# Optimization experiments

Hardware: AMD Instinct MI355X
Metric: run time of the kernel (lower is better)

## Reference

```python
import jax, jax.numpy as jnp
import numpy as np

EPS = 1e-06

def rmsnorm(x, w):
    x32 = x.astype(jnp.float32)
    var = jnp.mean(x32 * x32, axis=-1, keepdims=True)
    return w * (x32 * jax.lax.rsqrt(var + EPS)).astype(x.dtype)

def setup_inputs() -> dict:
    B, T, C = 16, 256, 16
    token_dim, text_dim = 1024, 512
    key = jax.random.key(0)
    ks = jax.random.split(key, 8)
    token_embeds = jax.random.normal(ks[0], (B, T, token_dim), dtype=jnp.float32)
    char_embeds = jax.random.normal(ks[1], (B, T, C, text_dim), dtype=jnp.float32)
    filler_embed = jax.random.normal(ks[2], (text_dim,), dtype=jnp.float32)
    mask = jax.random.randint(ks[3], (B, T, C), 0, 2).astype(bool)
    mask = mask.at[0].set(True)  # force max valid count == T*C (static output shape)
    token_ids_mask = jnp.ones((B, T), dtype=bool)
    # xavier-uniform-ish weights
    def xav(k, fan_out, fan_in, gain=1.0):
        lim = gain * np.sqrt(6.0 / (fan_in + fan_out))
        return jax.random.uniform(k, (fan_out, fan_in), jnp.float32, -lim, lim)
    W_down = xav(ks[4], text_dim, token_dim)
    W_proj = xav(ks[5], 3, text_dim, gain=0.2)
    W_fusion = xav(ks[6], text_dim, text_dim)
    w_pre = jnp.ones((token_dim,), jnp.float32)
    w_tok = jnp.ones((text_dim,), jnp.float32)
    w_char = jnp.ones((text_dim,), jnp.float32)
    return {"token_embeds": token_embeds, "token_ids_mask": token_ids_mask,
            "char_embeds": char_embeds, "char_ids_mask": mask,
            "filler_embed": filler_embed, "w_pre": w_pre, "w_tok": w_tok,
            "w_char": w_char, "W_down": W_down, "W_proj": W_proj,
            "W_fusion": W_fusion, "max_valid_chars": T * C}

def reference(token_embeds, token_ids_mask, char_embeds, char_ids_mask,
              filler_embed, w_pre, w_tok, w_char, W_down, W_proj, W_fusion,
              max_valid_chars):
    B, T, C, d = char_embeds.shape
    MV = int(max_valid_chars)
    tok = rmsnorm(token_embeds, w_pre)                       # [B,T,token_dim]
    feats = rmsnorm(jnp.einsum('btk,dk->btd', tok, W_down), w_tok)  # [B,T,d]
    params = jnp.einsum('btd,pd->btp', jax.nn.silu(feats), W_proj)  # [B,T,3]
    scale = params[..., 0][:, :, None, None]                 # [B,T,1,1]
    shift = params[..., 1][:, :, None, None]
    gate = jax.nn.sigmoid(params[..., 2][:, :, None, None])
    cn = rmsnorm(char_embeds, w_char)                        # [B,T,C,d]
    fused = jnp.einsum('btcd,ed->btce', jax.nn.silu(cn * (1.0 + scale) + shift), W_fusion)
    fused = gate * fused + (1.0 - gate) * cn                 # [B,T,C,d]
    flat = fused.reshape(B, T * C, d)
    m = char_ids_mask.reshape(B, T * C).astype(jnp.int32)
    pos = jnp.cumsum(m, axis=1) - 1                          # dest within row
    offs = jnp.arange(B, dtype=jnp.int32)[:, None] * MV
    idx = jnp.where(m > 0, offs + pos, B * MV)               # invalid -> dump slot
    buf = jnp.broadcast_to(filler_embed, (B * MV + 1, d))
    buf = buf.at[idx.reshape(-1)].set(flat.reshape(-1, d))
    return buf[: B * MV].reshape(B, MV, d)
```

## Files before the change

kernel.cpp:

```cpp
#include <hip/hip_runtime.h>
#include <cstdint>
#include <cstddef>

#define EPS 1e-6f

typedef short bf16x8 __attribute__((ext_vector_type(8)));
typedef float f32x4  __attribute__((ext_vector_type(4)));

__device__ __forceinline__ short f2bf(float x) {
    uint32_t u = __builtin_bit_cast(uint32_t, x);
    return (short)((u + 0x7FFFu + ((u >> 16) & 1u)) >> 16);
}
__device__ __forceinline__ float bf2f(short s) {
    uint32_t u = ((uint32_t)(uint16_t)s) << 16;
    return __builtin_bit_cast(float, u);
}

__global__ __launch_bounds__(256) void k_scan(const void* __restrict__ maskp,
                                              int* __restrict__ v_list,
                                              int* __restrict__ counts) {
    __shared__ int sc[256];
    __shared__ int mode_s;
    const int tid = threadIdx.x;
    const int b = blockIdx.x;
    const uint32_t* mi = (const uint32_t*)maskp;

    if (tid == 0) mode_s = 0;
    __syncthreads();
    int bad = 0;
    for (int k = tid; k < 1024; k += 256) bad |= (mi[k] > 1u) ? 1 : 0;
    if (bad) mode_s = 1;
    __syncthreads();

    int m[16];
    if (mode_s) {
        const uint4 v = *(const uint4*)((const uint8_t*)maskp + (b << 12) + tid * 16);
        const uint32_t ws[4] = {v.x, v.y, v.z, v.w};
#pragma unroll
        for (int w4 = 0; w4 < 4; ++w4)
#pragma unroll
            for (int e = 0; e < 4; ++e)
                m[w4 * 4 + e] = ((ws[w4] >> (8 * e)) & 0xffu) ? 1 : 0;
    } else {
        const uint32_t* p = mi + (b << 12) + tid * 16;
#pragma unroll
        for (int q = 0; q < 16; ++q) m[q] = p[q] ? 1 : 0;
    }
    int cl = 0;
#pragma unroll
    for (int q = 0; q < 16; ++q) cl += m[q];
    sc[tid] = cl;
    __syncthreads();
    for (int off = 1; off < 256; off <<= 1) {
        int v = sc[tid];
        int a = (tid >= off) ? sc[tid - off] : 0;
        __syncthreads();
        sc[tid] = v + a;
        __syncthreads();
    }
    int pos = sc[tid] - cl;
#pragma unroll
    for (int q = 0; q < 16; ++q) {
        if (m[q]) v_list[(b << 12) + pos++] = tid * 16 + q;
    }
    if (tid == 255) counts[b] = sc[255];
}

__global__ __launch_bounds__(256) void k_conv2(
    const float* __restrict__ s1, short* __restrict__ d1, int n1,
    const float* __restrict__ s2, short* __restrict__ d2, int n2) {
    const int gid = blockIdx.x * 256 + threadIdx.x;
    const float* src; short* dst; int idx;
    if (gid < n1) { src = s1; dst = d1; idx = gid; }
    else if (gid < n1 + n2) { src = s2; dst = d2; idx = gid - n1; }
    else return;
    const float4 v = ((const float4*)src)[idx];
    short4 o;
    o.x = f2bf(v.x); o.y = f2bf(v.y); o.z = f2bf(v.z); o.w = f2bf(v.w);
    ((short4*)dst)[idx] = o;
}

__global__ __launch_bounds__(256) void k_tokprep(const float* __restrict__ tokens,
                                                 const float* __restrict__ w_pre,
                                                 short* __restrict__ tokbf) {
    const int tid = threadIdx.x, lane = tid & 63, wave = tid >> 6;
    const int row = blockIdx.x * 4 + wave;
    const float* xp = tokens + (size_t)row * 1024 + lane * 16;
    float4 x[4];
#pragma unroll
    for (int q = 0; q < 4; ++q) x[q] = *(const float4*)&xp[q * 4];
    float ss = 0.f;
#pragma unroll
    for (int q = 0; q < 4; ++q)
        ss += x[q].x * x[q].x + x[q].y * x[q].y + x[q].z * x[q].z + x[q].w * x[q].w;
#pragma unroll
    for (int off = 32; off > 0; off >>= 1) ss += __shfl_down(ss, off);
    ss = __shfl(ss, 0);
    const float r = rsqrtf(ss * (1.0f / 1024.0f) + EPS);
    const float* wp = w_pre + lane * 16;
    short* op = tokbf + (size_t)row * 1024 + lane * 16;
#pragma unroll
    for (int h = 0; h < 2; ++h) {
        bf16x8 o;
#pragma unroll
        for (int q = 0; q < 2; ++q) {
            const float4 wv = *(const float4*)&wp[h * 8 + q * 4];
            const float4 xv = x[h * 2 + q];
            o[q * 4 + 0] = f2bf(xv.x * wv.x * r);
            o[q * 4 + 1] = f2bf(xv.y * wv.y * r);
            o[q * 4 + 2] = f2bf(xv.z * wv.z * r);
            o[q * 4 + 3] = f2bf(xv.w * wv.w * r);
        }
        *(bf16x8*)&op[h * 8] = o;
    }
}

__global__ __launch_bounds__(256) void k_gemm_tok(const short* __restrict__ tokbf,
                                                  const short* __restrict__ Wdbf,
                                                  float* __restrict__ feats) {
    __shared__ short As[128 * 32];
    __shared__ short Bs[64 * 32];
    const int tid = threadIdx.x, lane = tid & 63, w = tid >> 6;
    const int mt = blockIdx.x >> 3, nt = blockIdx.x & 7;
    const int wm = w >> 1, wn = w & 1;
    const short* hA = tokbf + (size_t)mt * 128 * 1024;
    const short* wB = Wdbf + (size_t)nt * 64 * 1024;

    f32x4 acc[4][2];
#pragma unroll
    for (int mi = 0; mi < 4; ++mi)
#pragma unroll
        for (int ni = 0; ni < 2; ++ni) acc[mi][ni] = (f32x4)0.f;

    const int rA = lane & 15, q8 = (lane >> 4) * 8;
    for (int kk = 0; kk < 1024; kk += 32) {
#pragma unroll
        for (int q = 0; q < 2; ++q) {
            const int cid = (w * 2 + q) * 64 + lane;
            const int r = cid >> 2, kc = cid & 3;
            __builtin_amdgcn_global_load_lds(
                (const __attribute__((address_space(1))) uint32_t*)(hA + (size_t)r * 1024 + kk + kc * 8),
                (__attribute__((address_space(3))) uint32_t*)&As[(w * 2 + q) * 512], 16, 0, 0);
        }
        {
            const int cid = tid;
            const int r = cid >> 2, kc = cid & 3;
            __builtin_amdgcn_global_load_lds(
                (const __attribute__((address_space(1))) uint32_t*)(wB + (size_t)r * 1024 + kk + kc * 8),
                (__attribute__((address_space(3))) uint32_t*)&Bs[w * 512], 16, 0, 0);
        }
        __syncthreads();
        bf16x8 af[4], bfr[2];
#pragma unroll
        for (int mi = 0; mi < 4; ++mi)
            af[mi] = *(const bf16x8*)&As[(wm * 64 + mi * 16 + rA) * 32 + q8];
#pragma unroll
        for (int ni = 0; ni < 2; ++ni)
            bfr[ni] = *(const bf16x8*)&Bs[(wn * 32 + ni * 16 + rA) * 32 + q8];
#pragma unroll
        for (int mi = 0; mi < 4; ++mi)
#pragma unroll
            for (int ni = 0; ni < 2; ++ni)
                acc[mi][ni] = __builtin_amdgcn_mfma_f32_16x16x32_bf16(af[mi], bfr[ni], acc[mi][ni], 0, 0, 0);
        __syncthreads();
    }
    const int rowb = mt * 128 + wm * 64 + (lane >> 4) * 4;
    const int colb = nt * 64 + wn * 32 + (lane & 15);
#pragma unroll
    for (int mi = 0; mi < 4; ++mi)
#pragma unroll
        for (int ni = 0; ni < 2; ++ni)
#pragma unroll
            for (int rg = 0; rg < 4; ++rg)
                feats[(size_t)(rowb + mi * 16 + rg) * 512 + colb + ni * 16] = acc[mi][ni][rg];
}

__global__ __launch_bounds__(64) void k_params(
    const float* __restrict__ feats_pre, const float* __restrict__ w_tok,
    const float* __restrict__ W_proj, float* __restrict__ params) {
    const int tk = blockIdx.x;
    const int lane = threadIdx.x;
    const int d0 = lane * 8;
    const float* fp = feats_pre + (size_t)tk * 512 + d0;
    const float4 f0 = *(const float4*)&fp[0];
    const float4 f1 = *(const float4*)&fp[4];
    float ss = f0.x * f0.x + f0.y * f0.y + f0.z * f0.z + f0.w * f0.w
             + f1.x * f1.x + f1.y * f1.y + f1.z * f1.z + f1.w * f1.w;
#pragma unroll
    for (int off = 32; off > 0; off >>= 1) ss += __shfl_down(ss, off);
    ss = __shfl(ss, 0);
    const float rms = rsqrtf(ss * (1.0f / 512.0f) + EPS);

    const float4 wt0 = *(const float4*)&w_tok[d0];
    const float4 wt1 = *(const float4*)&w_tok[d0 + 4];
    float fv[8] = {f0.x, f0.y, f0.z, f0.w, f1.x, f1.y, f1.z, f1.w};
    float wv[8] = {wt0.x, wt0.y, wt0.z, wt0.w, wt1.x, wt1.y, wt1.z, wt1.w};
    float s[8];
#pragma unroll
    for (int j = 0; j < 8; ++j) {
        const float v = fv[j] * wv[j] * rms;
        s[j] = v / (1.0f + expf(-v));
    }
    float p[3];
#pragma unroll
    for (int q = 0; q < 3; ++q) {
        const float* Wp = W_proj + (size_t)q * 512 + d0;
        const float4 a = *(const float4*)&Wp[0];
        const float4 c = *(const float4*)&Wp[4];
        p[q] = s[0] * a.x + s[1] * a.y + s[2] * a.z + s[3] * a.w
             + s[4] * c.x + s[5] * c.y + s[6] * c.z + s[7] * c.w;
#pragma unroll
        for (int off = 32; off > 0; off >>= 1) p[q] += __shfl_down(p[q], off);
    }
    if (lane == 0) {
        float* po = params + (size_t)tk * 4;
        po[0] = 1.0f + p[0];
        po[1] = p[1];
        po[2] = 1.0f / (1.0f + expf(-p[2]));
    }
}

__global__ __launch_bounds__(256) void k_prep(
    const float* __restrict__ chars, const float* __restrict__ w_char,
    const float* __restrict__ params, const int* __restrict__ v_list,
    const int* __restrict__ counts, short* __restrict__ hb,
    short* __restrict__ cnp, float* __restrict__ g_l) {
    const int tid = threadIdx.x, lane = tid & 63, wave = tid >> 6;
    const int b = blockIdx.x >> 10;
    const int j = (blockIdx.x & 1023) * 4 + wave;
    const int cnt = counts[b];
    const int cpad = (cnt + 127) & ~127;
    if (j >= cpad) return;
    short* hrow = hb + ((size_t)(b << 12) + j) * 512 + lane * 8;
    if (j >= cnt) {
        *(bf16x8*)hrow = (bf16x8)0;
        return;
    }
    const int i = v_list[(b << 12) + j];
    const float* xp = chars + ((size_t)(b << 12) + i) * 512 + lane * 8;
    const float4 x0 = *(const float4*)&xp[0];
    const float4 x1 = *(const float4*)&xp[4];
    float ss = x0.x * x0.x + x0.y * x0.y + x0.z * x0.z + x0.w * x0.w
             + x1.x * x1.x + x1.y * x1.y + x1.z * x1.z + x1.w * x1.w;
#pragma unroll
    for (int off = 32; off > 0; off >>= 1) ss += __shfl_down(ss, off);
    ss = __shfl(ss, 0);
    const float rms = rsqrtf(ss * (1.0f / 512.0f) + EPS);
    const float* pp = params + (size_t)((b << 8) + (i >> 4)) * 4;
    const float s1 = pp[0], sh = pp[1], g = pp[2];
    const float4 w0 = *(const float4*)&w_char[lane * 8];
    const float4 w1 = *(const float4*)&w_char[lane * 8 + 4];
    float xv[8] = {x0.x, x0.y, x0.z, x0.w, x1.x, x1.y, x1.z, x1.w};
    float wv[8] = {w0.x, w0.y, w0.z, w0.w, w1.x, w1.y, w1.z, w1.w};
    bf16x8 oh, oc;
    const float gm1 = 1.0f - g;
#pragma unroll
    for (int q = 0; q < 8; ++q) {
        const float cn = wv[q] * xv[q] * rms;
        const float a = cn * s1 + sh;
        oh[q] = f2bf(a / (1.0f + expf(-a)));
        oc[q] = f2bf(gm1 * cn);
    }
    *(bf16x8*)hrow = oh;
    *(bf16x8*)(cnp + ((size_t)(b << 12) + j) * 512 + lane * 8) = oc;
    if (lane == 0) g_l[(b << 12) + j] = g;
}

__global__ __launch_bounds__(256) void k_fill(
    const float* __restrict__ filler, const int* __restrict__ counts,
    float* __restrict__ out) {
    const int gid = blockIdx.x * 256 + threadIdx.x;
    const size_t e4 = (size_t)gid * 4;
    const int slot = gid >> 7;
    const int b = slot >> 12;
    const int j = slot & 4095;
    if (j >= counts[b]) {
        const int e0 = (int)(e4 & 511);
        *(float4*)&out[e4] = *(const float4*)&filler[e0];
    }
}

__global__ __launch_bounds__(256) void k_gemm_fus(
    const short* __restrict__ hb, const short* __restrict__ Wbf,
    const short* __restrict__ cnp, const float* __restrict__ g_l,
    const int* __restrict__ counts, float* __restrict__ out) {
    __shared__ union SM {
        struct { short A[128 * 32]; short B[128 * 32]; } ab;
        float ep[32][132];
    } sm;
    __shared__ float g_s[128];
    const int tid = threadIdx.x, lane = tid & 63, w = tid >> 6;
    const int b = blockIdx.x >> 7;
    const int mt = (blockIdx.x >> 2) & 31;
    const int nt = blockIdx.x & 3;
    const int cnt = counts[b];
    const int row0 = mt * 128;
    if (row0 >= cnt) return;
    const int wm = w >> 1, wn = w & 1;

    if (tid < 128) {
        const int j = row0 + tid;
        g_s[tid] = (j < cnt) ? g_l[(b << 12) + j] : 0.f;
    }

    const short* hA = hb + ((size_t)(b << 12) + row0) * 512;
    const short* wB = Wbf + (size_t)nt * 128 * 512;

    f32x4 acc[4][4];
#pragma unroll
    for (int mi = 0; mi < 4; ++mi)
#pragma unroll
        for (int ni = 0; ni < 4; ++ni) acc[mi][ni] = (f32x4)0.f;

    const int rA = lane & 15, q8 = (lane >> 4) * 8;
    for (int kk = 0; kk < 512; kk += 32) {
#pragma unroll
        for (int q = 0; q < 2; ++q) {
            const int cid = (w * 2 + q) * 64 + lane;
            const int r = cid >> 2, kc = cid & 3;
            const size_t go = (size_t)r * 512 + kk + kc * 8;
            __builtin_amdgcn_global_load_lds(
                (const __attribute__((address_space(1))) uint32_t*)(hA + go),
                (__attribute__((address_space(3))) uint32_t*)&sm.ab.A[(w * 2 + q) * 512], 16, 0, 0);
            __builtin_amdgcn_global_load_lds(
                (const __attribute__((address_space(1))) uint32_t*)(wB + go),
                (__attribute__((address_space(3))) uint32_t*)&sm.ab.B[(w * 2 + q) * 512], 16, 0, 0);
        }
        __syncthreads();
        bf16x8 af[4], bfr[4];
#pragma unroll
        for (int mi = 0; mi < 4; ++mi)
            af[mi] = *(const bf16x8*)&sm.ab.A[(wm * 64 + mi * 16 + rA) * 32 + q8];
#pragma unroll
        for (int ni = 0; ni < 4; ++ni)
            bfr[ni] = *(const bf16x8*)&sm.ab.B[(wn * 64 + ni * 16 + rA) * 32 + q8];
#pragma unroll
        for (int mi = 0; mi < 4; ++mi)
#pragma unroll
            for (int ni = 0; ni < 4; ++ni)
                acc[mi][ni] = __builtin_amdgcn_mfma_f32_16x16x32_bf16(af[mi], bfr[ni], acc[mi][ni], 0, 0, 0);
        __syncthreads();
    }

    const int r5 = tid >> 3;
    const int c0 = (tid & 7) * 16;
    const int cg = nt * 128 + c0;
#pragma unroll
    for (int mi = 0; mi < 4; ++mi) {
#pragma unroll
        for (int ni = 0; ni < 4; ++ni)
#pragma unroll
            for (int rg = 0; rg < 4; ++rg)
                sm.ep[wm * 16 + (lane >> 4) * 4 + rg][wn * 64 + ni * 16 + (lane & 15)] = acc[mi][ni][rg];
        __syncthreads();
        const int jl = (r5 < 16) ? (mi * 16 + r5) : (64 + mi * 16 + (r5 - 16));
        const int j = row0 + jl;
        if (j < cnt) {
            const float g = g_s[jl];
            const short* cp = cnp + ((size_t)(b << 12) + j) * 512 + cg;
            const bf16x8 cv0 = *(const bf16x8*)cp;
            const bf16x8 cv1 = *(const bf16x8*)(cp + 8);
            float cn16[16];
#pragma unroll
            for (int e = 0; e < 8; ++e) { cn16[e] = bf2f(cv0[e]); cn16[8 + e] = bf2f(cv1[e]); }
            float* op = out + ((size_t)(b << 12) + j) * 512 + cg;
#pragma unroll
            for (int q = 0; q < 4; ++q) {
                float4 o;
                o.x = g * sm.ep[r5][c0 + q * 4 + 0] + cn16[q * 4 + 0];
                o.y = g * sm.ep[r5][c0 + q * 4 + 1] + cn16[q * 4 + 1];
                o.z = g * sm.ep[r5][c0 + q * 4 + 2] + cn16[q * 4 + 2];
                o.w = g * sm.ep[r5][c0 + q * 4 + 3] + cn16[q * 4 + 3];
                *(float4*)&op[q * 4] = o;
            }
        }
        __syncthreads();
    }
}

extern "C" void kernel_launch(void* const* d_in, const int* in_sizes, int n_in,
                              void* d_out, int out_size, void* d_ws, size_t ws_size,
                              hipStream_t stream) {
    const float* tokens = (const float*)d_in[0];
    const float* chars  = (const float*)d_in[2];
    const void*  cmask  = d_in[3];
    const float* filler = (const float*)d_in[4];
    const float* w_pre  = (const float*)d_in[5];
    const float* w_tok  = (const float*)d_in[6];
    const float* w_char = (const float*)d_in[7];
    const float* W_down = (const float*)d_in[8];
    const float* W_proj = (const float*)d_in[9];
    const float* W_fus  = (const float*)d_in[10];
    float* out = (float*)d_out;

    float* feats_pre = (float*)d_ws;
    float* params    = feats_pre + (size_t)4096 * 512;
    int*   counts    = (int*)(params + (size_t)4096 * 4);
    int*   v_list    = counts + 16;
    float* g_l       = (float*)(v_list + 65536);
    short* Wbf       = (short*)(g_l + 65536);
    short* Wdbf      = Wbf + (size_t)512 * 512;
    short* tokbf     = Wdbf + (size_t)512 * 1024;
    short* hb        = tokbf + (size_t)4096 * 1024;
    short* cnp       = hb + (size_t)16 * 4096 * 512;

    k_scan<<<16, 256, 0, stream>>>(cmask, v_list, counts);
    k_conv2<<<768, 256, 0, stream>>>(W_fus, Wbf, 65536, W_down, Wdbf, 131072);
    k_tokprep<<<1024, 256, 0, stream>>>(tokens, w_pre, tokbf);
    k_gemm_tok<<<256, 256, 0, stream>>>(tokbf, Wdbf, feats_pre);
    k_params<<<4096, 64, 0, stream>>>(feats_pre, w_tok, W_proj, params);
    k_prep<<<16384, 256, 0, stream>>>(chars, w_char, params, v_list, counts, hb, cnp, g_l);
    k_fill<<<32768, 256, 0, stream>>>(filler, counts, out);
    k_gemm_fus<<<2048, 256, 0, stream>>>(hb, Wbf, cnp, g_l, counts, out);
}
```

Baseline: 403.4 us.

## Fuse filler writes into fusion GEMM and merge scan with weight conversion

Removes the separate fill kernel, which wrote the full 128 MB output for invalid slots. Tiles past the valid count now write filler directly inside the fusion GEMM, and tail rows of partial tiles get filler in the epilogue. The scan and weight-conversion kernels are merged into one launch. The block index is also remapped so neighbouring blocks share N tiles, and the epilogue uses strided float4 columns with a padded LDS stride to cut bank conflicts. Each output element is now written only once, at the cost of more epilogue branching.

```diff
diff --git a/kernel.cpp b/kernel.cpp
--- a/kernel.cpp
+++ b/kernel.cpp
@@ -16,12 +16,26 @@
     return __builtin_bit_cast(float, u);
 }
 
-__global__ __launch_bounds__(256) void k_scan(const void* __restrict__ maskp,
-                                              int* __restrict__ v_list,
-                                              int* __restrict__ counts) {
+__global__ __launch_bounds__(256) void k_scan_conv(
+    const void* __restrict__ maskp, int* __restrict__ v_list,
+    int* __restrict__ counts,
+    const float* __restrict__ s1, short* __restrict__ d1, int n1,
+    const float* __restrict__ s2, short* __restrict__ d2, int n2) {
+    const int tid = threadIdx.x;
+    if (blockIdx.x >= 16) {
+        const int gid = (blockIdx.x - 16) * 256 + tid;
+        const float* src; short* dst; int idx;
+        if (gid < n1) { src = s1; dst = d1; idx = gid; }
+        else if (gid < n1 + n2) { src = s2; dst = d2; idx = gid - n1; }
+        else return;
+        const float4 v = ((const float4*)src)[idx];
+        short4 o;
+        o.x = f2bf(v.x); o.y = f2bf(v.y); o.z = f2bf(v.z); o.w = f2bf(v.w);
+        ((short4*)dst)[idx] = o;
+        return;
+    }
     __shared__ int sc[256];
     __shared__ int mode_s;
-    const int tid = threadIdx.x;
     const int b = blockIdx.x;
     const uint32_t* mi = (const uint32_t*)maskp;
 
@@ -64,20 +78,6 @@
         if (m[q]) v_list[(b << 12) + pos++] = tid * 16 + q;
     }
     if (tid == 255) counts[b] = sc[255];
-}
-
-__global__ __launch_bounds__(256) void k_conv2(
-    const float* __restrict__ s1, short* __restrict__ d1, int n1,
-    const float* __restrict__ s2, short* __restrict__ d2, int n2) {
-    const int gid = blockIdx.x * 256 + threadIdx.x;
-    const float* src; short* dst; int idx;
-    if (gid < n1) { src = s1; dst = d1; idx = gid; }
-    else if (gid < n1 + n2) { src = s2; dst = d2; idx = gid - n1; }
-    else return;
-    const float4 v = ((const float4*)src)[idx];
-    short4 o;
-    o.x = f2bf(v.x); o.y = f2bf(v.y); o.z = f2bf(v.z); o.w = f2bf(v.w);
-    ((short4*)dst)[idx] = o;
 }
 
 __global__ __launch_bounds__(256) void k_tokprep(const float* __restrict__ tokens,
@@ -143,8 +143,7 @@
                 (__attribute__((address_space(3))) uint32_t*)&As[(w * 2 + q) * 512], 16, 0, 0);
         }
         {
-            const int cid = tid;
-            const int r = cid >> 2, kc = cid & 3;
+            const int r = tid >> 2, kc = tid & 3;
             __builtin_amdgcn_global_load_lds(
                 (const __attribute__((address_space(1))) uint32_t*)(wB + (size_t)r * 1024 + kk + kc * 8),
                 (__attribute__((address_space(3))) uint32_t*)&Bs[w * 512], 16, 0, 0);
@@ -266,36 +265,42 @@
     if (lane == 0) g_l[(b << 12) + j] = g;
 }
 
-__global__ __launch_bounds__(256) void k_fill(
-    const float* __restrict__ filler, const int* __restrict__ counts,
-    float* __restrict__ out) {
-    const int gid = blockIdx.x * 256 + threadIdx.x;
-    const size_t e4 = (size_t)gid * 4;
-    const int slot = gid >> 7;
-    const int b = slot >> 12;
-    const int j = slot & 4095;
-    if (j >= counts[b]) {
-        const int e0 = (int)(e4 & 511);
-        *(float4*)&out[e4] = *(const float4*)&filler[e0];
-    }
-}
-
 __global__ __launch_bounds__(256) void k_gemm_fus(
     const short* __restrict__ hb, const short* __restrict__ Wbf,
     const short* __restrict__ cnp, const float* __restrict__ g_l,
-    const int* __restrict__ counts, float* __restrict__ out) {
+    const float* __restrict__ filler, const int* __restrict__ counts,
+    float* __restrict__ out) {
     __shared__ union SM {
         struct { short A[128 * 32]; short B[128 * 32]; } ab;
-        float ep[32][132];
+        float ep[32][140];
     } sm;
     __shared__ float g_s[128];
     const int tid = threadIdx.x, lane = tid & 63, w = tid >> 6;
-    const int b = blockIdx.x >> 7;
-    const int mt = (blockIdx.x >> 2) & 31;
-    const int nt = blockIdx.x & 3;
+    const int low3 = blockIdx.x & 7;
+    const int rest = blockIdx.x >> 3;
+    const int nt = rest & 3;
+    const int g = ((rest >> 2) << 3) | low3;
+    const int b = g >> 5;
+    const int mt = g & 31;
     const int cnt = counts[b];
     const int row0 = mt * 128;
-    if (row0 >= cnt) return;
+    const int r5 = tid >> 3;
+    const int c0 = (tid & 7) * 4;
+    const int cgb = nt * 128;
+
+    if (row0 >= cnt) {
+        float4 flr[4];
+#pragma unroll
+        for (int q = 0; q < 4; ++q) flr[q] = *(const float4*)&filler[cgb + c0 + q * 32];
+#pragma unroll
+        for (int rr = 0; rr < 4; ++rr) {
+            const int j = row0 + rr * 32 + r5;
+            float* op = out + ((size_t)(b << 12) + j) * 512 + cgb + c0;
+#pragma unroll
+            for (int q = 0; q < 4; ++q) *(float4*)&op[q * 32] = flr[q];
+        }
+        return;
+    }
     const int wm = w >> 1, wn = w & 1;
 
     if (tid < 128) {
@@ -342,9 +347,6 @@
         __syncthreads();
     }
 
-    const int r5 = tid >> 3;
-    const int c0 = (tid & 7) * 16;
-    const int cg = nt * 128 + c0;
 #pragma unroll
     for (int mi = 0; mi < 4; ++mi) {
 #pragma unroll
@@ -355,24 +357,25 @@
         __syncthreads();
         const int jl = (r5 < 16) ? (mi * 16 + r5) : (64 + mi * 16 + (r5 - 16));
         const int j = row0 + jl;
+        float* op = out + ((size_t)(b << 12) + j) * 512 + cgb + c0;
         if (j < cnt) {
-            const float g = g_s[jl];
-            const short* cp = cnp + ((size_t)(b << 12) + j) * 512 + cg;
-            const bf16x8 cv0 = *(const bf16x8*)cp;
-            const bf16x8 cv1 = *(const bf16x8*)(cp + 8);
-            float cn16[16];
-#pragma unroll
-            for (int e = 0; e < 8; ++e) { cn16[e] = bf2f(cv0[e]); cn16[8 + e] = bf2f(cv1[e]); }
-            float* op = out + ((size_t)(b << 12) + j) * 512 + cg;
+            const float gg = g_s[jl];
+            const short* cp = cnp + ((size_t)(b << 12) + j) * 512 + cgb + c0;
 #pragma unroll
             for (int q = 0; q < 4; ++q) {
+                const short4 cv = *(const short4*)(cp + q * 32);
+                const float4 e = *(const float4*)&sm.ep[r5][c0 + q * 32];
                 float4 o;
-                o.x = g * sm.ep[r5][c0 + q * 4 + 0] + cn16[q * 4 + 0];
-                o.y = g * sm.ep[r5][c0 + q * 4 + 1] + cn16[q * 4 + 1];
-                o.z = g * sm.ep[r5][c0 + q * 4 + 2] + cn16[q * 4 + 2];
-                o.w = g * sm.ep[r5][c0 + q * 4 + 3] + cn16[q * 4 + 3];
-                *(float4*)&op[q * 4] = o;
+                o.x = gg * e.x + bf2f(cv.x);
+                o.y = gg * e.y + bf2f(cv.y);
+                o.z = gg * e.z + bf2f(cv.z);
+                o.w = gg * e.w + bf2f(cv.w);
+                *(float4*)&op[q * 32] = o;
             }
+        } else {
+#pragma unroll
+            for (int q = 0; q < 4; ++q)
+                *(float4*)&op[q * 32] = *(const float4*)&filler[cgb + c0 + q * 32];
         }
         __syncthreads();
     }
@@ -404,12 +407,11 @@
     short* hb        = tokbf + (size_t)4096 * 1024;
     short* cnp       = hb + (size_t)16 * 4096 * 512;
 
-    k_scan<<<16, 256, 0, stream>>>(cmask, v_list, counts);
-    k_conv2<<<768, 256, 0, stream>>>(W_fus, Wbf, 65536, W_down, Wdbf, 131072);
+    k_scan_conv<<<784, 256, 0, stream>>>(cmask, v_list, counts,
+                                         W_fus, Wbf, 65536, W_down, Wdbf, 131072);
     k_tokprep<<<1024, 256, 0, stream>>>(tokens, w_pre, tokbf);
     k_gemm_tok<<<256, 256, 0, stream>>>(tokbf, Wdbf, feats_pre);
     k_params<<<4096, 64, 0, stream>>>(feats_pre, w_tok, W_proj, params);
     k_prep<<<16384, 256, 0, stream>>>(chars, w_char, params, v_list, counts, hb, cnp, g_l);
-    k_fill<<<32768, 256, 0, stream>>>(filler, counts, out);
-    k_gemm_fus<<<2048, 256, 0, stream>>>(hb, Wbf, cnp, g_l, counts, out);
-}
+    k_gemm_fus<<<2048, 256, 0, stream>>>(hb, Wbf, cnp, g_l, filler, counts, out);
+}
```

After: 387.2 us. 4.0% less time.
